# Kernel optimization log

Measured on AMD Instinct MI355X. Metric: run time of the kernel, lower is better.

## Reference

```python
import jax, jax.numpy as jnp
import numpy as np

NUM_EMBEDDINGS = 1024
EMBEDDING_DIM = 64
COMMITMENT_COST = 0.25
DECAY = 0.99
EPSILON = 1e-05


def setup_inputs() -> dict:
    key = jax.random.key(0)
    k1, k2 = jax.random.split(key)
    inputs = jax.random.normal(k1, (32, EMBEDDING_DIM, 32, 32), dtype=jnp.float32)
    # torch init: uniform(-1/N, 1/N)
    lim = 1.0 / NUM_EMBEDDINGS
    weight = jax.random.uniform(k2, (NUM_EMBEDDINGS, EMBEDDING_DIM), dtype=jnp.float32,
                                minval=-lim, maxval=lim)
    ema_cluster_size = jnp.zeros((NUM_EMBEDDINGS,), dtype=jnp.float32)
    ema_w = weight  # buffer initialized as a clone of the weight
    return {"inputs": inputs, "weight": weight,
            "ema_cluster_size": ema_cluster_size, "ema_w": ema_w}


def reference(inputs, weight, ema_cluster_size, ema_w):
    B, D, H, W = inputs.shape
    N = weight.shape[0]
    # [B, D, H, W] -> [B*H*W, D]
    flat = jnp.transpose(inputs, (0, 2, 3, 1)).reshape(-1, D)

    # squared L2 distances to every codebook entry: [B*H*W, N]
    distances = (jnp.sum(flat ** 2, axis=1, keepdims=True)
                 + jnp.sum(weight ** 2, axis=1)
                 - 2.0 * jnp.matmul(flat, weight.T))
    indices = jnp.argmin(distances, axis=1)  # [B*H*W]

    quantized_flat = weight[indices]  # gather, [B*H*W, D]
    quantized = jnp.transpose(quantized_flat.reshape(B, H, W, D), (0, 3, 1, 2))

    # --- EMA codebook update (training mode, no_grad in torch) ---
    counts = jax.ops.segment_sum(jnp.ones_like(indices, dtype=jnp.float32),
                                 indices, num_segments=N)  # == one_hot sum
    new_ema_cluster_size = DECAY * ema_cluster_size + (1.0 - DECAY) * counts
    n_total = jnp.sum(new_ema_cluster_size)
    cluster_size = ((new_ema_cluster_size + EPSILON)
                    / (n_total + N * EPSILON) * n_total)
    dw = jax.ops.segment_sum(flat, indices, num_segments=N)  # == encodings.T @ flat
    new_ema_w = DECAY * ema_w + (1.0 - DECAY) * dw
    new_weight = new_ema_w / cluster_size[:, None]

    # commitment loss (detached quantized)
    commitment_loss = jnp.mean((jax.lax.stop_gradient(quantized) - inputs) ** 2)
    vq_loss = COMMITMENT_COST * commitment_loss

    # straight-through estimator
    quantized_st = inputs + jax.lax.stop_gradient(quantized - inputs)

    avg_probs = counts / flat.shape[0]
    perplexity = jnp.exp(-jnp.sum(avg_probs * jnp.log(avg_probs + 1e-10)))

    return (quantized_st, vq_loss, indices.reshape(B, H, W), perplexity,
            new_ema_cluster_size, new_ema_w, new_weight)
```

## Files before the change

### kernel.cpp

```cpp
#include <hip/hip_runtime.h>
#include <math.h>

typedef _Float16 half8 __attribute__((ext_vector_type(8)));
typedef _Float16 half4v __attribute__((ext_vector_type(4)));
typedef float    f32x4 __attribute__((ext_vector_type(4)));

#define O_Q     0
#define O_LOSS  2097152
#define O_IDX   2097153
#define O_PERP  2129921
#define O_NECS  2129922
#define O_EMAW  2130946
#define O_W     2196482

#define W_WBF    0
#define W_SW2    65536
#define W_RSQ    66560
#define W_CNT    132096
#define W_DW     133120
#define W_LOSS   198656
#define W_ZN     66561

#define F16_MIN_NORM 6.103515625e-05f

__global__ __launch_bounds__(256)
void k_prep(const float* __restrict__ w, const float* __restrict__ x,
            _Float16* __restrict__ wbf, float* __restrict__ wsq,
            float* __restrict__ rsq, float* __restrict__ zbase) {
    __shared__ float sh[64][65];
    int tid = threadIdx.x, blk = blockIdx.x;

    for (int z = blk * 256 + tid; z < W_ZN; z += 256 * 256) zbase[z] = 0.f;

    if (blk < 64) {
        int T  = blk * 256 + tid;
        int ct = T >> 8, j = (T >> 6) & 3, l = T & 63;
        int kb = j & 1, isLo = j >> 1;
        int c  = ct * 16 + (l & 15), g = l >> 4;
        half8 o;
        #pragma unroll
        for (int e = 0; e < 8; ++e) {
            int kd = kb * 32 + g * 4 + (e & 3) + ((e >> 2) << 4);
            float wv = w[c * 64 + kd];
            _Float16 h = (fabsf(wv) >= F16_MIN_NORM) ? (_Float16)wv : (_Float16)0.f;
            if (isLo) {
                float hf = (float)h;
                o[e] = (_Float16)((wv - hf) * 16384.0f);
            } else {
                o[e] = h;
            }
        }
        *(half8*)(wbf + ((ct * 4 + j) * 64 + l) * 8) = o;
    }

    if (blk < 16) {
        int j0 = blk * 64;
        for (int p = 0; p < 16; ++p) {
            int f = p * 256 + tid;
            int j = f >> 6, d = f & 63;
            sh[j][d] = w[(j0 + j) * 64 + d];
        }
        __syncthreads();
        if (tid < 64) {
            double s = 0.0;
            #pragma unroll
            for (int d = 0; d < 64; ++d) {
                double v = (double)sh[tid][d];
                s = fma(v, v, s);
            }
            wsq[j0 + tid] = (float)s;
        }
    }

    if (blk >= 128) {
        int r = (blk - 128) * 256 + tid;
        const float* xp = x + (r >> 10) * 65536 + (r & 1023);
        double s = 0.0;
        #pragma unroll 8
        for (int d = 0; d < 64; ++d) {
            double v = (double)xp[d * 1024];
            s = fma(v, v, s);
        }
        rsq[r] = (float)s;
    }
}

__global__ __launch_bounds__(512, 8)
void k_dist(const float* __restrict__ x, const _Float16* __restrict__ wbf,
            const float* __restrict__ wsq, const float* __restrict__ rsq_g,
            const float* __restrict__ w,
            float* __restrict__ out_idxf,
            float* __restrict__ outq, float* __restrict__ counts,
            float* __restrict__ dw, float* __restrict__ loss) {
    __shared__ _Float16 xhi[64 * 32];
    __shared__ _Float16 xlo[64 * 32];
    __shared__ float x32[32][65];
    __shared__ float q32[32][65];
    __shared__ float bvs[8][16];
    __shared__ int   bis[8][16];
    __shared__ int   idxl[32];
    __shared__ float red[8];
    int tid = threadIdx.x;
    int rbase = blockIdx.x * 32;
    int b = rbase >> 10, hw0 = rbase & 1023;
    const float* xb = x + b * 65536 + hw0;

    {
        int d = tid >> 3, r4 = (tid & 7) << 2;
        float4 v = *(const float4*)(xb + d * 1024 + r4);
        float vv[4] = {v.x, v.y, v.z, v.w};
        half4v h, lo;
        #pragma unroll
        for (int q = 0; q < 4; ++q) {
            float xv = vv[q];
            _Float16 hh = (fabsf(xv) >= F16_MIN_NORM) ? (_Float16)xv : (_Float16)0.f;
            h[q]  = hh;
            lo[q] = (_Float16)((xv - (float)hh) * 2048.0f);
            x32[r4 + q][d] = xv;
        }
        *(half4v*)&xhi[d * 32 + r4] = h;
        *(half4v*)&xlo[d * 32 + r4] = lo;
    }
    __syncthreads();

    int l   = tid & 63;
    int wid = tid >> 6;
    int ctq = wid & 3;
    int rt  = wid >> 2;
    int g = l >> 4, n16 = l & 15;
    int m = rt * 16 + n16;

    half8 ahi[2], alo[2];
    #pragma unroll
    for (int kb = 0; kb < 2; ++kb) {
        #pragma unroll
        for (int e = 0; e < 8; ++e) {
            int kd = kb * 32 + g * 4 + (e & 3) + ((e >> 2) << 4);
            ahi[kb][e] = xhi[kd * 32 + m];
            alo[kb][e] = xlo[kd * 32 + m];
        }
    }

    float rq[4];
    #pragma unroll
    for (int i = 0; i < 4; ++i) rq[i] = rsq_g[rbase + rt * 16 + g * 4 + i];

    float best[4];
    int   bidx[4];
    #pragma unroll
    for (int i = 0; i < 4; ++i) { best[i] = 3.4e38f; bidx[i] = 0; }

    const half8* wv8 = (const half8*)wbf;
    #pragma unroll 1
    for (int c8 = 0; c8 < 16; ++c8) {
        int ct = ctq * 16 + c8;
        const half8* wb = wv8 + ct * 256 + l;
        half8 bh0 = wb[0], bh1 = wb[64], bl0 = wb[128], bl1 = wb[192];
        float wsqv = wsq[ct * 16 + n16];
        int n = ct * 16 + n16;

        f32x4 c1 = {0.f, 0.f, 0.f, 0.f};
        f32x4 c2 = {0.f, 0.f, 0.f, 0.f};
        f32x4 c3 = {0.f, 0.f, 0.f, 0.f};
        c1 = __builtin_amdgcn_mfma_f32_16x16x32_f16(ahi[0], bh0, c1, 0, 0, 0);
        c1 = __builtin_amdgcn_mfma_f32_16x16x32_f16(ahi[1], bh1, c1, 0, 0, 0);
        c2 = __builtin_amdgcn_mfma_f32_16x16x32_f16(alo[0], bh0, c2, 0, 0, 0);
        c2 = __builtin_amdgcn_mfma_f32_16x16x32_f16(alo[1], bh1, c2, 0, 0, 0);
        c3 = __builtin_amdgcn_mfma_f32_16x16x32_f16(ahi[0], bl0, c3, 0, 0, 0);
        c3 = __builtin_amdgcn_mfma_f32_16x16x32_f16(ahi[1], bl1, c3, 0, 0, 0);

        #pragma unroll
        for (int i = 0; i < 4; ++i) {
            float dot = fmaf(c2[i], 4.8828125e-4f, c1[i]);
            dot = fmaf(c3[i], 6.103515625e-05f, dot);
            float t1 = rq[i] + wsqv;
            float sc = fmaf(dot, -2.0f, t1);
            if (sc < best[i]) { best[i] = sc; bidx[i] = n; }
        }
    }

    #pragma unroll
    for (int off = 1; off < 16; off <<= 1) {
        #pragma unroll
        for (int i = 0; i < 4; ++i) {
            float ov = __shfl_xor(best[i], off);
            int   oi = __shfl_xor(bidx[i], off);
            if (ov < best[i] || (ov == best[i] && oi < bidx[i])) {
                best[i] = ov; bidx[i] = oi;
            }
        }
    }
    if (n16 == 0) {
        #pragma unroll
        for (int i = 0; i < 4; ++i) {
            bvs[wid][g * 4 + i] = best[i];
            bis[wid][g * 4 + i] = bidx[i];
        }
    }
    __syncthreads();

    if (tid < 32) {
        int r16 = tid & 15, rh = tid >> 4;
        float bb = bvs[rh * 4][r16]; int ii = bis[rh * 4][r16];
        #pragma unroll
        for (int q = 1; q < 4; ++q) {
            float ov = bvs[rh * 4 + q][r16]; int oi = bis[rh * 4 + q][r16];
            if (ov < bb) { bb = ov; ii = oi; }
        }
        idxl[tid] = ii;
        out_idxf[rbase + tid] = (float)ii;
        atomicAdd(&counts[ii], 1.0f);
    }
    __syncthreads();

    {
        int n  = wid * 4 + (l >> 4);
        int d4 = (l & 15) << 2;
        *(float4*)&q32[n][d4] = *(const float4*)(w + idxl[n] * 64 + d4);
    }
    __syncthreads();

    float ll = 0.f;
    #pragma unroll
    for (int p = 0; p < 4; ++p) {
        int e = p * 512 + tid;
        int nn = e & 31, d = e >> 5;
        float q  = q32[nn][d];
        float xv = x32[nn][d];
        float dd = q - xv;
        ll += dd * dd;
        outq[b * 65536 + d * 1024 + hw0 + nn] = q;
    }
    #pragma unroll
    for (int off = 32; off; off >>= 1) ll += __shfl_down(ll, off);
    if (l == 0) red[wid] = ll;
    __syncthreads();
    if (tid == 0) {
        float s = 0.f;
        #pragma unroll
        for (int i = 0; i < 8; ++i) s += red[i];
        atomicAdd(loss, s);
    }

    #pragma unroll
    for (int v = 0; v < 4; ++v) {
        int n = wid * 4 + v;
        atomicAdd(&dw[idxl[n] * 64 + l], x32[n][l]);
    }
}

__global__ __launch_bounds__(256)
void k_final(const float* __restrict__ ema_cs, const float* __restrict__ ema_w,
             const float* __restrict__ counts, const float* __restrict__ dw,
             const float* __restrict__ loss, float* __restrict__ out) {
    __shared__ float cs[1024];
    __shared__ float redA[4], redB[4];
    int tid = threadIdx.x;

    float necs[4];
    float s1 = 0.f, s2 = 0.f;
    #pragma unroll
    for (int q = 0; q < 4; ++q) {
        int j = q * 256 + tid;
        float c  = counts[j];
        float ne = 0.99f * ema_cs[j] + 0.01f * c;
        necs[q] = ne;
        float p = c * (1.0f / 32768.0f);
        s1 += ne;
        s2 += -p * logf(p + 1e-10f);
    }
    #pragma unroll
    for (int off = 32; off; off >>= 1) {
        s1 += __shfl_down(s1, off);
        s2 += __shfl_down(s2, off);
    }
    if ((tid & 63) == 0) { redA[tid >> 6] = s1; redB[tid >> 6] = s2; }
    __syncthreads();
    float ntot = redA[0] + redA[1] + redA[2] + redA[3];
    #pragma unroll
    for (int q = 0; q < 4; ++q)
        cs[q * 256 + tid] = (necs[q] + 1e-5f) / (ntot + 1024.0f * 1e-5f) * ntot;

    if (blockIdx.x == 0) {
        #pragma unroll
        for (int q = 0; q < 4; ++q) out[O_NECS + q * 256 + tid] = necs[q];
        if (tid == 0) {
            out[O_PERP] = expf(redB[0] + redB[1] + redB[2] + redB[3]);
            out[O_LOSS] = 0.25f * loss[0] * (1.0f / 2097152.0f);
        }
    }
    __syncthreads();

    int f = blockIdx.x * 256 + tid;
    int j = f >> 6;
    float ne = 0.99f * ema_w[f] + 0.01f * dw[f];
    out[O_EMAW + f] = ne;
    out[O_W + f]    = ne / cs[j];
}

extern "C" void kernel_launch(void* const* d_in, const int* in_sizes, int n_in,
                              void* d_out, int out_size, void* d_ws, size_t ws_size,
                              hipStream_t stream) {
    const float* x      = (const float*)d_in[0];
    const float* w      = (const float*)d_in[1];
    const float* ema_cs = (const float*)d_in[2];
    const float* ema_w  = (const float*)d_in[3];
    float* out = (float*)d_out;
    float* ws  = (float*)d_ws;

    _Float16* wbf  = (_Float16*)(ws + W_WBF);
    float* wsq     = ws + W_SW2;
    float* rsqb    = ws + W_RSQ;
    float* counts  = ws + W_CNT;
    float* dwb     = ws + W_DW;
    float* lossb   = ws + W_LOSS;

    k_prep <<<256,  256, 0, stream>>>(w, x, wbf, wsq, rsqb, counts);
    k_dist <<<1024, 512, 0, stream>>>(x, wbf, wsq, rsqb, w,
                                      out + O_IDX, out + O_Q, counts, dwb, lossb);
    k_final<<<256,  256, 0, stream>>>(ema_cs, ema_w, counts, dwb, lossb, out);
}
```

Measured before the change: 51.95 us.

## Double rows per block and keep codebook fragments in registers across row tiles

The distance kernel now handles 64 rows per block instead of 32, using half as many blocks. Each wave loads the fp16 hi/lo codebook fragments for four column tiles into registers once per pass and reuses them across four row tiles, while the split x fragments are staged in shared memory in MFMA-ready layout. The goal is to cut repeated global/L2 loads of the codebook per row. In exchange it uses more registers and shared memory (launch bounds drop to 4 blocks per CU), leaves fewer blocks to fill the GPU, and adds a two-pass merge of per-wave minima.

```diff
diff --git a/kernel.cpp b/kernel.cpp
--- a/kernel.cpp
+++ b/kernel.cpp
@@ -85,127 +85,147 @@
     }
 }
 
-__global__ __launch_bounds__(512, 8)
+__global__ __launch_bounds__(512, 4)
 void k_dist(const float* __restrict__ x, const _Float16* __restrict__ wbf,
             const float* __restrict__ wsq, const float* __restrict__ rsq_g,
             const float* __restrict__ w,
             float* __restrict__ out_idxf,
             float* __restrict__ outq, float* __restrict__ counts,
             float* __restrict__ dw, float* __restrict__ loss) {
-    __shared__ _Float16 xhi[64 * 32];
-    __shared__ _Float16 xlo[64 * 32];
-    __shared__ float x32[32][65];
-    __shared__ float q32[32][65];
-    __shared__ float bvs[8][16];
-    __shared__ int   bis[8][16];
-    __shared__ int   idxl[32];
+    __shared__ _Float16 xfh[4][2][64][8];
+    __shared__ _Float16 xfl[4][2][64][8];
+    __shared__ float x32[64][65];
+    __shared__ float q32[64][65];
+    __shared__ float bvs[8][64];
+    __shared__ int   bis[8][64];
+    __shared__ int   idxl[64];
     __shared__ float red[8];
     int tid = threadIdx.x;
-    int rbase = blockIdx.x * 32;
+    int rbase = blockIdx.x * 64;
     int b = rbase >> 10, hw0 = rbase & 1023;
     const float* xb = x + b * 65536 + hw0;
 
-    {
-        int d = tid >> 3, r4 = (tid & 7) << 2;
-        float4 v = *(const float4*)(xb + d * 1024 + r4);
-        float vv[4] = {v.x, v.y, v.z, v.w};
-        half4v h, lo;
-        #pragma unroll
-        for (int q = 0; q < 4; ++q) {
-            float xv = vv[q];
-            _Float16 hh = (fabsf(xv) >= F16_MIN_NORM) ? (_Float16)xv : (_Float16)0.f;
-            h[q]  = hh;
-            lo[q] = (_Float16)((xv - (float)hh) * 2048.0f);
-            x32[r4 + q][d] = xv;
-        }
-        *(half4v*)&xhi[d * 32 + r4] = h;
-        *(half4v*)&xlo[d * 32 + r4] = lo;
-    }
-    __syncthreads();
-
     int l   = tid & 63;
     int wid = tid >> 6;
-    int ctq = wid & 3;
-    int rt  = wid >> 2;
     int g = l >> 4, n16 = l & 15;
-    int m = rt * 16 + n16;
-
-    half8 ahi[2], alo[2];
-    #pragma unroll
-    for (int kb = 0; kb < 2; ++kb) {
+
+    #pragma unroll
+    for (int p = 0; p < 2; ++p) {
+        int f = p * 512 + tid;
+        int d = f >> 4, r4 = (f & 15) << 2;
+        float4 v = *(const float4*)(xb + d * 1024 + r4);
+        x32[r4 + 0][d] = v.x;
+        x32[r4 + 1][d] = v.y;
+        x32[r4 + 2][d] = v.z;
+        x32[r4 + 3][d] = v.w;
+    }
+    __syncthreads();
+
+    {
+        int frt = tid >> 7, fkb = (tid >> 6) & 1, fl = tid & 63;
+        int fn16 = fl & 15, fg = fl >> 4;
+        int row = frt * 16 + fn16;
+        half8 oh, ol;
         #pragma unroll
         for (int e = 0; e < 8; ++e) {
-            int kd = kb * 32 + g * 4 + (e & 3) + ((e >> 2) << 4);
-            ahi[kb][e] = xhi[kd * 32 + m];
-            alo[kb][e] = xlo[kd * 32 + m];
-        }
-    }
-
-    float rq[4];
-    #pragma unroll
-    for (int i = 0; i < 4; ++i) rq[i] = rsq_g[rbase + rt * 16 + g * 4 + i];
-
-    float best[4];
-    int   bidx[4];
-    #pragma unroll
-    for (int i = 0; i < 4; ++i) { best[i] = 3.4e38f; bidx[i] = 0; }
+            int kd = fkb * 32 + fg * 4 + (e & 3) + ((e >> 2) << 4);
+            float xv = x32[row][kd];
+            _Float16 hh = (fabsf(xv) >= F16_MIN_NORM) ? (_Float16)xv : (_Float16)0.f;
+            oh[e] = hh;
+            ol[e] = (_Float16)((xv - (float)hh) * 2048.0f);
+        }
+        *(half8*)&xfh[frt][fkb][fl][0] = oh;
+        *(half8*)&xfl[frt][fkb][fl][0] = ol;
+    }
+    __syncthreads();
 
     const half8* wv8 = (const half8*)wbf;
+
     #pragma unroll 1
-    for (int c8 = 0; c8 < 16; ++c8) {
-        int ct = ctq * 16 + c8;
-        const half8* wb = wv8 + ct * 256 + l;
-        half8 bh0 = wb[0], bh1 = wb[64], bl0 = wb[128], bl1 = wb[192];
-        float wsqv = wsq[ct * 16 + n16];
-        int n = ct * 16 + n16;
-
-        f32x4 c1 = {0.f, 0.f, 0.f, 0.f};
-        f32x4 c2 = {0.f, 0.f, 0.f, 0.f};
-        f32x4 c3 = {0.f, 0.f, 0.f, 0.f};
-        c1 = __builtin_amdgcn_mfma_f32_16x16x32_f16(ahi[0], bh0, c1, 0, 0, 0);
-        c1 = __builtin_amdgcn_mfma_f32_16x16x32_f16(ahi[1], bh1, c1, 0, 0, 0);
-        c2 = __builtin_amdgcn_mfma_f32_16x16x32_f16(alo[0], bh0, c2, 0, 0, 0);
-        c2 = __builtin_amdgcn_mfma_f32_16x16x32_f16(alo[1], bh1, c2, 0, 0, 0);
-        c3 = __builtin_amdgcn_mfma_f32_16x16x32_f16(ahi[0], bl0, c3, 0, 0, 0);
-        c3 = __builtin_amdgcn_mfma_f32_16x16x32_f16(ahi[1], bl1, c3, 0, 0, 0);
-
-        #pragma unroll
-        for (int i = 0; i < 4; ++i) {
-            float dot = fmaf(c2[i], 4.8828125e-4f, c1[i]);
-            dot = fmaf(c3[i], 6.103515625e-05f, dot);
-            float t1 = rq[i] + wsqv;
-            float sc = fmaf(dot, -2.0f, t1);
-            if (sc < best[i]) { best[i] = sc; bidx[i] = n; }
-        }
-    }
-
-    #pragma unroll
-    for (int off = 1; off < 16; off <<= 1) {
-        #pragma unroll
-        for (int i = 0; i < 4; ++i) {
-            float ov = __shfl_xor(best[i], off);
-            int   oi = __shfl_xor(bidx[i], off);
-            if (ov < best[i] || (ov == best[i] && oi < bidx[i])) {
-                best[i] = ov; bidx[i] = oi;
-            }
-        }
-    }
-    if (n16 == 0) {
-        #pragma unroll
-        for (int i = 0; i < 4; ++i) {
-            bvs[wid][g * 4 + i] = best[i];
-            bis[wid][g * 4 + i] = bidx[i];
-        }
-    }
-    __syncthreads();
-
-    if (tid < 32) {
-        int r16 = tid & 15, rh = tid >> 4;
-        float bb = bvs[rh * 4][r16]; int ii = bis[rh * 4][r16];
-        #pragma unroll
-        for (int q = 1; q < 4; ++q) {
-            float ov = bvs[rh * 4 + q][r16]; int oi = bis[rh * 4 + q][r16];
-            if (ov < bb) { bb = ov; ii = oi; }
+    for (int p = 0; p < 2; ++p) {
+        half8 bh0[4], bh1[4], bl0[4], bl1[4];
+        float wsqv[4];
+        int ctb = p * 32 + wid * 4;
+        #pragma unroll
+        for (int c = 0; c < 4; ++c) {
+            const half8* wbp = wv8 + (ctb + c) * 256 + l;
+            bh0[c] = wbp[0]; bh1[c] = wbp[64];
+            bl0[c] = wbp[128]; bl1[c] = wbp[192];
+            wsqv[c] = wsq[(ctb + c) * 16 + n16];
+        }
+
+        #pragma unroll 1
+        for (int rt = 0; rt < 4; ++rt) {
+            half8 ah0 = *(const half8*)&xfh[rt][0][l][0];
+            half8 ah1 = *(const half8*)&xfh[rt][1][l][0];
+            half8 al0 = *(const half8*)&xfl[rt][0][l][0];
+            half8 al1 = *(const half8*)&xfl[rt][1][l][0];
+            float rq[4];
+            #pragma unroll
+            for (int i = 0; i < 4; ++i)
+                rq[i] = rsq_g[rbase + rt * 16 + g * 4 + i];
+
+            float best[4];
+            int   bidx[4];
+            #pragma unroll
+            for (int i = 0; i < 4; ++i) { best[i] = 3.4e38f; bidx[i] = 0; }
+
+            #pragma unroll
+            for (int c = 0; c < 4; ++c) {
+                int ct = ctb + c;
+                int n = ct * 16 + n16;
+                f32x4 c1 = {0.f, 0.f, 0.f, 0.f};
+                f32x4 c2 = {0.f, 0.f, 0.f, 0.f};
+                f32x4 c3 = {0.f, 0.f, 0.f, 0.f};
+                c1 = __builtin_amdgcn_mfma_f32_16x16x32_f16(ah0, bh0[c], c1, 0, 0, 0);
+                c1 = __builtin_amdgcn_mfma_f32_16x16x32_f16(ah1, bh1[c], c1, 0, 0, 0);
+                c2 = __builtin_amdgcn_mfma_f32_16x16x32_f16(al0, bh0[c], c2, 0, 0, 0);
+                c2 = __builtin_amdgcn_mfma_f32_16x16x32_f16(al1, bh1[c], c2, 0, 0, 0);
+                c3 = __builtin_amdgcn_mfma_f32_16x16x32_f16(ah0, bl0[c], c3, 0, 0, 0);
+                c3 = __builtin_amdgcn_mfma_f32_16x16x32_f16(ah1, bl1[c], c3, 0, 0, 0);
+
+                #pragma unroll
+                for (int i = 0; i < 4; ++i) {
+                    float dot = fmaf(c2[i], 4.8828125e-4f, c1[i]);
+                    dot = fmaf(c3[i], 6.103515625e-05f, dot);
+                    float t1 = rq[i] + wsqv[c];
+                    float sc = fmaf(dot, -2.0f, t1);
+                    if (sc < best[i]) { best[i] = sc; bidx[i] = n; }
+                }
+            }
+
+            #pragma unroll
+            for (int off = 1; off < 16; off <<= 1) {
+                #pragma unroll
+                for (int i = 0; i < 4; ++i) {
+                    float ov = __shfl_xor(best[i], off);
+                    int   oi = __shfl_xor(bidx[i], off);
+                    if (ov < best[i] || (ov == best[i] && oi < bidx[i])) {
+                        best[i] = ov; bidx[i] = oi;
+                    }
+                }
+            }
+            if (n16 == 0) {
+                #pragma unroll
+                for (int i = 0; i < 4; ++i) {
+                    int slot = rt * 16 + g * 4 + i;
+                    if (p == 0) {
+                        bvs[wid][slot] = best[i]; bis[wid][slot] = bidx[i];
+                    } else if (best[i] < bvs[wid][slot]) {
+                        bvs[wid][slot] = best[i]; bis[wid][slot] = bidx[i];
+                    }
+                }
+            }
+        }
+    }
+    __syncthreads();
+
+    if (tid < 64) {
+        float bb = bvs[0][tid]; int ii = bis[0][tid];
+        #pragma unroll
+        for (int q = 1; q < 8; ++q) {
+            float ov = bvs[q][tid]; int oi = bis[q][tid];
+            if (ov < bb || (ov == bb && oi < ii)) { bb = ov; ii = oi; }
         }
         idxl[tid] = ii;
         out_idxf[rbase + tid] = (float)ii;
@@ -213,8 +233,9 @@
     }
     __syncthreads();
 
-    {
-        int n  = wid * 4 + (l >> 4);
+    #pragma unroll
+    for (int v = 0; v < 2; ++v) {
+        int n  = wid * 8 + v * 4 + (l >> 4);
         int d4 = (l & 15) << 2;
         *(float4*)&q32[n][d4] = *(const float4*)(w + idxl[n] * 64 + d4);
     }
@@ -222,9 +243,9 @@
 
     float ll = 0.f;
     #pragma unroll
-    for (int p = 0; p < 4; ++p) {
+    for (int p = 0; p < 8; ++p) {
         int e = p * 512 + tid;
-        int nn = e & 31, d = e >> 5;
+        int nn = e & 63, d = e >> 6;
         float q  = q32[nn][d];
         float xv = x32[nn][d];
         float dd = q - xv;
@@ -243,8 +264,8 @@
     }
 
     #pragma unroll
-    for (int v = 0; v < 4; ++v) {
-        int n = wid * 4 + v;
+    for (int v = 0; v < 8; ++v) {
+        int n = wid * 8 + v;
         atomicAdd(&dw[idxl[n] * 64 + l], x32[n][l]);
     }
 }
@@ -315,8 +336,8 @@
     float* dwb     = ws + W_DW;
     float* lossb   = ws + W_LOSS;
 
-    k_prep <<<256,  256, 0, stream>>>(w, x, wbf, wsq, rsqb, counts);
-    k_dist <<<1024, 512, 0, stream>>>(x, wbf, wsq, rsqb, w,
-                                      out + O_IDX, out + O_Q, counts, dwb, lossb);
-    k_final<<<256,  256, 0, stream>>>(ema_cs, ema_w, counts, dwb, lossb, out);
+    k_prep <<<256, 256, 0, stream>>>(w, x, wbf, wsq, rsqb, counts);
+    k_dist <<<512, 512, 0, stream>>>(x, wbf, wsq, rsqb, w,
+                                     out + O_IDX, out + O_Q, counts, dwb, lossb);
+    k_final<<<256, 256, 0, stream>>>(ema_cs, ema_w, counts, dwb, lossb, out);
 }
```

Measured after the change: 53.14 us. 2.3% more time.

## Enlarge distance tile to 128 rows per block and fuse row-norm computation

Applied to the files above, without the earlier changes.

Each k_dist block now handles 128 rows instead of 32. Each wave owns 16 rows and scans all 1024 codes with a software-prefetched codebook load, with periodic block barriers to keep waves in step. The row squared-norm pass moves out of k_prep into shared memory inside k_dist, and the cross-wave argmin reduction is removed. The aim is to cut repeated codebook reads and the extra x read, at the cost of a 4x smaller grid (256 blocks), heavier shared memory use and lower occupancy.

```diff
diff --git a/kernel.cpp b/kernel.cpp
--- a/kernel.cpp
+++ b/kernel.cpp
@@ -15,7 +15,6 @@
 
 #define W_WBF    0
 #define W_SW2    65536
-#define W_RSQ    66560
 #define W_CNT    132096
 #define W_DW     133120
 #define W_LOSS   198656
@@ -24,9 +23,9 @@
 #define F16_MIN_NORM 6.103515625e-05f
 
 __global__ __launch_bounds__(256)
-void k_prep(const float* __restrict__ w, const float* __restrict__ x,
+void k_prep(const float* __restrict__ w,
             _Float16* __restrict__ wbf, float* __restrict__ wsq,
-            float* __restrict__ rsq, float* __restrict__ zbase) {
+            float* __restrict__ zbase) {
     __shared__ float sh[64][65];
     int tid = threadIdx.x, blk = blockIdx.x;
 
@@ -71,42 +70,31 @@
             wsq[j0 + tid] = (float)s;
         }
     }
-
-    if (blk >= 128) {
-        int r = (blk - 128) * 256 + tid;
-        const float* xp = x + (r >> 10) * 65536 + (r & 1023);
-        double s = 0.0;
-        #pragma unroll 8
-        for (int d = 0; d < 64; ++d) {
-            double v = (double)xp[d * 1024];
-            s = fma(v, v, s);
-        }
-        rsq[r] = (float)s;
-    }
 }
 
-__global__ __launch_bounds__(512, 8)
+__global__ __launch_bounds__(512, 2)
 void k_dist(const float* __restrict__ x, const _Float16* __restrict__ wbf,
-            const float* __restrict__ wsq, const float* __restrict__ rsq_g,
+            const float* __restrict__ wsq,
             const float* __restrict__ w,
             float* __restrict__ out_idxf,
             float* __restrict__ outq, float* __restrict__ counts,
             float* __restrict__ dw, float* __restrict__ loss) {
-    __shared__ _Float16 xhi[64 * 32];
-    __shared__ _Float16 xlo[64 * 32];
-    __shared__ float x32[32][65];
-    __shared__ float q32[32][65];
-    __shared__ float bvs[8][16];
-    __shared__ int   bis[8][16];
-    __shared__ int   idxl[32];
+    __shared__ _Float16 xhi[64 * 128];
+    __shared__ _Float16 xlo[64 * 128];
+    __shared__ float x32[128][65];
+    __shared__ float q32[128][65];
+    __shared__ float rsq[128];
+    __shared__ int   idxl[128];
     __shared__ float red[8];
     int tid = threadIdx.x;
-    int rbase = blockIdx.x * 32;
+    int rbase = blockIdx.x * 128;
     int b = rbase >> 10, hw0 = rbase & 1023;
     const float* xb = x + b * 65536 + hw0;
 
-    {
-        int d = tid >> 3, r4 = (tid & 7) << 2;
+    #pragma unroll
+    for (int p = 0; p < 4; ++p) {
+        int f = p * 512 + tid;
+        int d = f >> 5, r4 = (f & 31) << 2;
         float4 v = *(const float4*)(xb + d * 1024 + r4);
         float vv[4] = {v.x, v.y, v.z, v.w};
         half4v h, lo;
@@ -118,17 +106,25 @@
             lo[q] = (_Float16)((xv - (float)hh) * 2048.0f);
             x32[r4 + q][d] = xv;
         }
-        *(half4v*)&xhi[d * 32 + r4] = h;
-        *(half4v*)&xlo[d * 32 + r4] = lo;
-    }
-    __syncthreads();
+        *(half4v*)&xhi[d * 128 + r4] = h;
+        *(half4v*)&xlo[d * 128 + r4] = lo;
+    }
+    __syncthreads();
+
+    if (tid < 128) {
+        double s = 0.0;
+        #pragma unroll
+        for (int d = 0; d < 64; ++d) {
+            double v = (double)x32[tid][d];
+            s = fma(v, v, s);
+        }
+        rsq[tid] = (float)s;
+    }
 
     int l   = tid & 63;
     int wid = tid >> 6;
-    int ctq = wid & 3;
-    int rt  = wid >> 2;
     int g = l >> 4, n16 = l & 15;
-    int m = rt * 16 + n16;
+    int row = wid * 16 + n16;
 
     half8 ahi[2], alo[2];
     #pragma unroll
@@ -136,14 +132,15 @@
         #pragma unroll
         for (int e = 0; e < 8; ++e) {
             int kd = kb * 32 + g * 4 + (e & 3) + ((e >> 2) << 4);
-            ahi[kb][e] = xhi[kd * 32 + m];
-            alo[kb][e] = xlo[kd * 32 + m];
-        }
-    }
+            ahi[kb][e] = xhi[kd * 128 + row];
+            alo[kb][e] = xlo[kd * 128 + row];
+        }
+    }
+    __syncthreads();
 
     float rq[4];
     #pragma unroll
-    for (int i = 0; i < 4; ++i) rq[i] = rsq_g[rbase + rt * 16 + g * 4 + i];
+    for (int i = 0; i < 4; ++i) rq[i] = rsq[wid * 16 + g * 4 + i];
 
     float best[4];
     int   bidx[4];
@@ -151,12 +148,20 @@
     for (int i = 0; i < 4; ++i) { best[i] = 3.4e38f; bidx[i] = 0; }
 
     const half8* wv8 = (const half8*)wbf;
+
+    const half8* wp0 = wv8 + l;
+    half8 pbh0 = wp0[0], pbh1 = wp0[64], pbl0 = wp0[128], pbl1 = wp0[192];
+    float pwsq = wsq[n16];
+
     #pragma unroll 1
-    for (int c8 = 0; c8 < 16; ++c8) {
-        int ct = ctq * 16 + c8;
-        const half8* wb = wv8 + ct * 256 + l;
-        half8 bh0 = wb[0], bh1 = wb[64], bl0 = wb[128], bl1 = wb[192];
-        float wsqv = wsq[ct * 16 + n16];
+    for (int ct = 0; ct < 64; ++ct) {
+        half8 bh0 = pbh0, bh1 = pbh1, bl0 = pbl0, bl1 = pbl1;
+        float wsqv = pwsq;
+        if (ct < 63) {
+            const half8* wn = wv8 + (ct + 1) * 256 + l;
+            pbh0 = wn[0]; pbh1 = wn[64]; pbl0 = wn[128]; pbl1 = wn[192];
+            pwsq = wsq[(ct + 1) * 16 + n16];
+        }
         int n = ct * 16 + n16;
 
         f32x4 c1 = {0.f, 0.f, 0.f, 0.f};
@@ -177,6 +182,8 @@
             float sc = fmaf(dot, -2.0f, t1);
             if (sc < best[i]) { best[i] = sc; bidx[i] = n; }
         }
+
+        if ((ct & 3) == 3) __syncthreads();
     }
 
     #pragma unroll
@@ -193,28 +200,17 @@
     if (n16 == 0) {
         #pragma unroll
         for (int i = 0; i < 4; ++i) {
-            bvs[wid][g * 4 + i] = best[i];
-            bis[wid][g * 4 + i] = bidx[i];
-        }
-    }
-    __syncthreads();
-
-    if (tid < 32) {
-        int r16 = tid & 15, rh = tid >> 4;
-        float bb = bvs[rh * 4][r16]; int ii = bis[rh * 4][r16];
-        #pragma unroll
-        for (int q = 1; q < 4; ++q) {
-            float ov = bvs[rh * 4 + q][r16]; int oi = bis[rh * 4 + q][r16];
-            if (ov < bb) { bb = ov; ii = oi; }
-        }
-        idxl[tid] = ii;
-        out_idxf[rbase + tid] = (float)ii;
-        atomicAdd(&counts[ii], 1.0f);
-    }
-    __syncthreads();
-
-    {
-        int n  = wid * 4 + (l >> 4);
+            int rl = wid * 16 + g * 4 + i;
+            idxl[rl] = bidx[i];
+            out_idxf[rbase + rl] = (float)bidx[i];
+            atomicAdd(&counts[bidx[i]], 1.0f);
+        }
+    }
+    __syncthreads();
+
+    #pragma unroll
+    for (int v = 0; v < 4; ++v) {
+        int n  = wid * 16 + v * 4 + (l >> 4);
         int d4 = (l & 15) << 2;
         *(float4*)&q32[n][d4] = *(const float4*)(w + idxl[n] * 64 + d4);
     }
@@ -222,9 +218,9 @@
 
     float ll = 0.f;
     #pragma unroll
-    for (int p = 0; p < 4; ++p) {
+    for (int p = 0; p < 16; ++p) {
         int e = p * 512 + tid;
-        int nn = e & 31, d = e >> 5;
+        int nn = e & 127, d = e >> 7;
         float q  = q32[nn][d];
         float xv = x32[nn][d];
         float dd = q - xv;
@@ -243,8 +239,8 @@
     }
 
     #pragma unroll
-    for (int v = 0; v < 4; ++v) {
-        int n = wid * 4 + v;
+    for (int v = 0; v < 16; ++v) {
+        int n = wid * 16 + v;
         atomicAdd(&dw[idxl[n] * 64 + l], x32[n][l]);
     }
 }
@@ -310,13 +306,12 @@
 
     _Float16* wbf  = (_Float16*)(ws + W_WBF);
     float* wsq     = ws + W_SW2;
-    float* rsqb    = ws + W_RSQ;
     float* counts  = ws + W_CNT;
     float* dwb     = ws + W_DW;
     float* lossb   = ws + W_LOSS;
 
-    k_prep <<<256,  256, 0, stream>>>(w, x, wbf, wsq, rsqb, counts);
-    k_dist <<<1024, 512, 0, stream>>>(x, wbf, wsq, rsqb, w,
-                                      out + O_IDX, out + O_Q, counts, dwb, lossb);
-    k_final<<<256,  256, 0, stream>>>(ema_cs, ema_w, counts, dwb, lossb, out);
+    k_prep <<<256, 256, 0, stream>>>(w, wbf, wsq, counts);
+    k_dist <<<256, 512, 0, stream>>>(x, wbf, wsq, w,
+                                     out + O_IDX, out + O_Q, counts, dwb, lossb);
+    k_final<<<256, 256, 0, stream>>>(ema_cs, ema_w, counts, dwb, lossb, out);
 }
```

Result: slower. 59.65 us (+14.8%).
